# Optimization experiments

Hardware: AMD Instinct MI355X
Metric: run time of the kernel (lower is better)

## Reference

```python
import jax, jax.numpy as jnp
import numpy as np

B, N, C_IN = 8, 2048, 64
NUM_TERMS, NUM_CHANNELS = 3, 64
LN_EPS = 1e-5


def setup_inputs() -> dict:
    key = jax.random.key(0)
    k1, k2, k3 = jax.random.split(key, 3)
    A = jax.random.normal(k1, (B, N, N), dtype=jnp.float32) / jnp.sqrt(N).astype(jnp.float32)
    X = jax.random.normal(k2, (B, N, C_IN), dtype=jnp.float32)
    # xavier_uniform on h of shape [num_terms+1, num_channels, num_nodes]
    fan_in, fan_out = NUM_CHANNELS, N
    bound = float(np.sqrt(6.0 / (fan_in + fan_out)))
    h = jax.random.uniform(k3, (NUM_TERMS + 1, NUM_CHANNELS, N), dtype=jnp.float32,
                           minval=-bound, maxval=bound)
    gamma = jnp.ones((NUM_CHANNELS,), dtype=jnp.float32)
    beta = jnp.zeros((NUM_CHANNELS,), dtype=jnp.float32)
    return {"A": A, "X": X, "h": h, "gamma": gamma, "beta": beta}


def reference(A, X, h, gamma, beta):
    # Original loops compute: Y[b,n,c] = sum_i h[i,c,n] * (A^i @ sum_ch X[...,ch])[b,n]
    num_terms = h.shape[0] - 1
    Xs = X.sum(axis=-1)  # [B, N] -- inner channel loop collapses to a sum

    def step(p, _):
        p_next = jnp.einsum('bmn,bn->bm', A, p)  # A^i @ Xs
        return p_next, p_next

    _, Ps = jax.lax.scan(step, Xs, None, length=num_terms)  # [T, B, N]
    P = jnp.concatenate([Xs[None], Ps], axis=0)  # [T+1, B, N], P[0] = I @ Xs

    Y = jnp.einsum('icn,ibn->bnc', h, P)  # [B, N, C]

    mean = Y.mean(axis=-1, keepdims=True)
    var = Y.var(axis=-1, keepdims=True)
    Yn = (Y - mean) * jax.lax.rsqrt(var + LN_EPS) * gamma + beta
    return jnp.tanh(Yn)
```

## Files before the change

### kernel.cpp

```cpp
#include <hip/hip_runtime.h>
#include <hip/hip_bf16.h>
#include <hip/hip_fp16.h>
#include <math.h>

#define BB 8
#define NN 2048
#define C_IN 64
#define NCH 64
#define LN_EPS 1e-5f

__global__ void xsum_kernel(const float* __restrict__ X, float* __restrict__ Xs) {
    int row  = (blockIdx.x * blockDim.x + threadIdx.x) >> 6;
    int lane = threadIdx.x & 63;
    float v = X[(size_t)row * C_IN + lane];
    #pragma unroll
    for (int off = 32; off > 0; off >>= 1)
        v += __shfl_down(v, off, 64);
    if (lane == 0) Xs[row] = v;
}

__global__ __launch_bounds__(256, 4) void matvec_cvt_kernel(
        const float* __restrict__ A,
        const float* __restrict__ pin,
        float* __restrict__ pout,
        __half* __restrict__ A16) {
    const int b    = blockIdx.y;
    const int wave = threadIdx.x >> 6;
    const int lane = threadIdx.x & 63;
    const int m    = blockIdx.x * 4 + wave;

    const float4* pin4 = (const float4*)(pin + (size_t)b * NN);
    const float4* Ar   = (const float4*)(A + (size_t)b * NN * NN + (size_t)m * NN);

    float4 x[8], pr[8];
    #pragma unroll
    for (int j = 0; j < 8; ++j) x[j]  = Ar[j * 64 + lane];
    #pragma unroll
    for (int j = 0; j < 8; ++j) pr[j] = pin4[j * 64 + lane];

    float acc = 0.f;
    #pragma unroll
    for (int j = 0; j < 8; ++j)
        acc += x[j].x * pr[j].x + x[j].y * pr[j].y + x[j].z * pr[j].z + x[j].w * pr[j].w;

    float2* A16r = (float2*)(A16 + (size_t)b * NN * NN + (size_t)m * NN);
    #pragma unroll
    for (int j = 0; j < 8; ++j) {
        union { float2 f2; __half2 h2[2]; } u;
        u.h2[0] = __floats2half2_rn(x[j].x, x[j].y);
        u.h2[1] = __floats2half2_rn(x[j].z, x[j].w);
        A16r[j * 64 + lane] = u.f2;
    }

    #pragma unroll
    for (int off = 32; off > 0; off >>= 1)
        acc += __shfl_down(acc, off, 64);
    if (lane == 0) pout[(size_t)b * NN + m] = acc;
}

__global__ __launch_bounds__(256, 4) void matvec16_kernel(
        const __half* __restrict__ A16,
        const float* __restrict__ pin,
        float* __restrict__ pout) {
    const int b    = blockIdx.y;
    const int wave = threadIdx.x >> 6;
    const int lane = threadIdx.x & 63;
    const int m    = blockIdx.x * 4 + wave;

    const float4* pin4 = (const float4*)(pin + (size_t)b * NN);
    const float4* Ar   = (const float4*)(A16 + (size_t)b * NN * NN + (size_t)m * NN);

    float4 xr[4], pa[4], pb[4];
    #pragma unroll
    for (int j = 0; j < 4; ++j) xr[j] = Ar[j * 64 + lane];
    #pragma unroll
    for (int j = 0; j < 4; ++j) {
        pa[j] = pin4[2 * (j * 64 + lane)];
        pb[j] = pin4[2 * (j * 64 + lane) + 1];
    }

    float acc = 0.f;
    #pragma unroll
    for (int j = 0; j < 4; ++j) {
        const __half2* hx = (const __half2*)&xr[j];
        float2 f0 = __half22float2(hx[0]);
        float2 f1 = __half22float2(hx[1]);
        float2 f2 = __half22float2(hx[2]);
        float2 f3 = __half22float2(hx[3]);
        acc += f0.x * pa[j].x + f0.y * pa[j].y + f1.x * pa[j].z + f1.y * pa[j].w
             + f2.x * pb[j].x + f2.y * pb[j].y + f3.x * pb[j].z + f3.y * pb[j].w;
    }

    #pragma unroll
    for (int off = 32; off > 0; off >>= 1)
        acc += __shfl_down(acc, off, 64);
    if (lane == 0) pout[(size_t)b * NN + m] = acc;
}

__global__ __launch_bounds__(256, 4) void matvec16_ln_kernel(
        const __half* __restrict__ A16,
        const float* __restrict__ P,
        const float* __restrict__ h,
        const float* __restrict__ gamma,
        const float* __restrict__ beta,
        float* __restrict__ out) {
    const int b    = blockIdx.y;
    const int wave = threadIdx.x >> 6;
    const int lane = threadIdx.x & 63;
    const int n    = blockIdx.x * 4 + wave;

    const float4* pin4 = (const float4*)(P + (size_t)(2 * BB + b) * NN);
    const float4* Ar   = (const float4*)(A16 + (size_t)b * NN * NN + (size_t)n * NN);

    float4 xr[4], pa[4], pb[4];
    #pragma unroll
    for (int j = 0; j < 4; ++j) xr[j] = Ar[j * 64 + lane];
    #pragma unroll
    for (int j = 0; j < 4; ++j) {
        pa[j] = pin4[2 * (j * 64 + lane)];
        pb[j] = pin4[2 * (j * 64 + lane) + 1];
    }

    float acc = 0.f;
    #pragma unroll
    for (int j = 0; j < 4; ++j) {
        const __half2* hx = (const __half2*)&xr[j];
        float2 f0 = __half22float2(hx[0]);
        float2 f1 = __half22float2(hx[1]);
        float2 f2 = __half22float2(hx[2]);
        float2 f3 = __half22float2(hx[3]);
        acc += f0.x * pa[j].x + f0.y * pa[j].y + f1.x * pa[j].z + f1.y * pa[j].w
             + f2.x * pb[j].x + f2.y * pb[j].y + f3.x * pb[j].z + f3.y * pb[j].w;
    }
    #pragma unroll
    for (int off = 32; off > 0; off >>= 1)
        acc += __shfl_xor(acc, off, 64);
    const float p3 = acc;

    const int idx = b * NN + n;
    const float p0 = P[idx];
    const float p1 = P[BB * NN + idx];
    const float p2 = P[2 * BB * NN + idx];

    float y = h[(size_t)(0 * NCH + lane) * NN + n] * p0
            + h[(size_t)(1 * NCH + lane) * NN + n] * p1
            + h[(size_t)(2 * NCH + lane) * NN + n] * p2
            + h[(size_t)(3 * NCH + lane) * NN + n] * p3;

    float s = y;
    #pragma unroll
    for (int off = 32; off > 0; off >>= 1)
        s += __shfl_xor(s, off, 64);
    const float mean = s * (1.f / NCH);

    float d = y - mean;
    float vs = d * d;
    #pragma unroll
    for (int off = 32; off > 0; off >>= 1)
        vs += __shfl_xor(vs, off, 64);
    const float rstd = rsqrtf(vs * (1.f / NCH) + LN_EPS);

    out[(size_t)idx * NCH + lane] = tanhf(d * rstd * gamma[lane] + beta[lane]);
}

extern "C" void kernel_launch(void* const* d_in, const int* in_sizes, int n_in,
                              void* d_out, int out_size, void* d_ws, size_t ws_size,
                              hipStream_t stream) {
    const float* A     = (const float*)d_in[0];
    const float* X     = (const float*)d_in[1];
    const float* h     = (const float*)d_in[2];
    const float* gamma = (const float*)d_in[3];
    const float* beta  = (const float*)d_in[4];
    float* out = (float*)d_out;

    float*  P   = (float*)d_ws;
    __half* A16 = (__half*)((char*)d_ws + (1u << 20));

    dim3 mv_grid(NN / 4, BB);

    xsum_kernel<<<(BB * NN) / 4, 256, 0, stream>>>(X, P);

    matvec_cvt_kernel<<<mv_grid, 256, 0, stream>>>(A, P, P + BB * NN, A16);

    matvec16_kernel<<<mv_grid, 256, 0, stream>>>(
        A16, P + BB * NN, P + 2 * BB * NN);

    matvec16_ln_kernel<<<mv_grid, 256, 0, stream>>>(
        A16, P, h, gamma, beta, out);
}
```

Baseline: 247.0 us.

## Stage input vector in LDS and process four rows per wave with prefetch

Each block now loads the per-batch input vector once into shared memory and each wave handles four matrix rows instead of one, double-buffering the next row's loads in registers while computing the current one. The goal is to cut redundant global reads of the vector, which every wave previously fetched for itself, and to keep more memory requests in flight per wave. The cost is a quarter as many blocks in the grid, more registers per thread, and one block-wide sync.

```diff
diff --git a/kernel.cpp b/kernel.cpp
--- a/kernel.cpp
+++ b/kernel.cpp
@@ -24,77 +24,111 @@
         const float* __restrict__ pin,
         float* __restrict__ pout,
         __half* __restrict__ A16) {
-    const int b    = blockIdx.y;
+    __shared__ float4 p4[NN / 4];
+    const int b = blockIdx.y;
+
+    const float4* src = (const float4*)(pin + (size_t)b * NN);
+    p4[threadIdx.x]       = src[threadIdx.x];
+    p4[threadIdx.x + 256] = src[threadIdx.x + 256];
+    __syncthreads();
+
     const int wave = threadIdx.x >> 6;
     const int lane = threadIdx.x & 63;
-    const int m    = blockIdx.x * 4 + wave;
-
-    const float4* pin4 = (const float4*)(pin + (size_t)b * NN);
-    const float4* Ar   = (const float4*)(A + (size_t)b * NN * NN + (size_t)m * NN);
-
-    float4 x[8], pr[8];
-    #pragma unroll
-    for (int j = 0; j < 8; ++j) x[j]  = Ar[j * 64 + lane];
-    #pragma unroll
-    for (int j = 0; j < 8; ++j) pr[j] = pin4[j * 64 + lane];
-
-    float acc = 0.f;
-    #pragma unroll
-    for (int j = 0; j < 8; ++j)
-        acc += x[j].x * pr[j].x + x[j].y * pr[j].y + x[j].z * pr[j].z + x[j].w * pr[j].w;
-
-    float2* A16r = (float2*)(A16 + (size_t)b * NN * NN + (size_t)m * NN);
-    #pragma unroll
-    for (int j = 0; j < 8; ++j) {
-        union { float2 f2; __half2 h2[2]; } u;
-        u.h2[0] = __floats2half2_rn(x[j].x, x[j].y);
-        u.h2[1] = __floats2half2_rn(x[j].z, x[j].w);
-        A16r[j * 64 + lane] = u.f2;
-    }
-
-    #pragma unroll
-    for (int off = 32; off > 0; off >>= 1)
-        acc += __shfl_down(acc, off, 64);
-    if (lane == 0) pout[(size_t)b * NN + m] = acc;
+    const int m0   = blockIdx.x * 16 + wave * 4;
+    const float* Ab = A + (size_t)b * NN * NN;
+
+    float4 buf[2][8];
+    {
+        const float4* r = (const float4*)(Ab + (size_t)m0 * NN);
+        #pragma unroll
+        for (int j = 0; j < 8; ++j) buf[0][j] = r[j * 64 + lane];
+    }
+
+    #pragma unroll
+    for (int i = 0; i < 4; ++i) {
+        const int m = m0 + i;
+        if (i < 3) {
+            const float4* rn = (const float4*)(Ab + (size_t)(m + 1) * NN);
+            #pragma unroll
+            for (int j = 0; j < 8; ++j) buf[(i + 1) & 1][j] = rn[j * 64 + lane];
+        }
+
+        float acc = 0.f;
+        #pragma unroll
+        for (int j = 0; j < 8; ++j) {
+            float4 x  = buf[i & 1][j];
+            float4 pv = p4[j * 64 + lane];
+            acc += x.x * pv.x + x.y * pv.y + x.z * pv.z + x.w * pv.w;
+        }
+
+        float2* A16r = (float2*)(A16 + (size_t)b * NN * NN + (size_t)m * NN);
+        #pragma unroll
+        for (int j = 0; j < 8; ++j) {
+            union { float2 f2; __half2 h2[2]; } u;
+            u.h2[0] = __floats2half2_rn(buf[i & 1][j].x, buf[i & 1][j].y);
+            u.h2[1] = __floats2half2_rn(buf[i & 1][j].z, buf[i & 1][j].w);
+            A16r[j * 64 + lane] = u.f2;
+        }
+
+        #pragma unroll
+        for (int off = 32; off > 0; off >>= 1)
+            acc += __shfl_down(acc, off, 64);
+        if (lane == 0) pout[(size_t)b * NN + m] = acc;
+    }
 }
 
 __global__ __launch_bounds__(256, 4) void matvec16_kernel(
         const __half* __restrict__ A16,
         const float* __restrict__ pin,
         float* __restrict__ pout) {
-    const int b    = blockIdx.y;
+    __shared__ float4 p4[NN / 4];
+    const int b = blockIdx.y;
+
+    const float4* src = (const float4*)(pin + (size_t)b * NN);
+    p4[threadIdx.x]       = src[threadIdx.x];
+    p4[threadIdx.x + 256] = src[threadIdx.x + 256];
+    __syncthreads();
+
     const int wave = threadIdx.x >> 6;
     const int lane = threadIdx.x & 63;
-    const int m    = blockIdx.x * 4 + wave;
-
-    const float4* pin4 = (const float4*)(pin + (size_t)b * NN);
-    const float4* Ar   = (const float4*)(A16 + (size_t)b * NN * NN + (size_t)m * NN);
-
-    float4 xr[4], pa[4], pb[4];
-    #pragma unroll
-    for (int j = 0; j < 4; ++j) xr[j] = Ar[j * 64 + lane];
-    #pragma unroll
-    for (int j = 0; j < 4; ++j) {
-        pa[j] = pin4[2 * (j * 64 + lane)];
-        pb[j] = pin4[2 * (j * 64 + lane) + 1];
-    }
-
-    float acc = 0.f;
-    #pragma unroll
-    for (int j = 0; j < 4; ++j) {
-        const __half2* hx = (const __half2*)&xr[j];
-        float2 f0 = __half22float2(hx[0]);
-        float2 f1 = __half22float2(hx[1]);
-        float2 f2 = __half22float2(hx[2]);
-        float2 f3 = __half22float2(hx[3]);
-        acc += f0.x * pa[j].x + f0.y * pa[j].y + f1.x * pa[j].z + f1.y * pa[j].w
-             + f2.x * pb[j].x + f2.y * pb[j].y + f3.x * pb[j].z + f3.y * pb[j].w;
-    }
-
-    #pragma unroll
-    for (int off = 32; off > 0; off >>= 1)
-        acc += __shfl_down(acc, off, 64);
-    if (lane == 0) pout[(size_t)b * NN + m] = acc;
+    const int m0   = blockIdx.x * 16 + wave * 4;
+    const __half* Ab = A16 + (size_t)b * NN * NN;
+
+    float4 buf[2][4];
+    {
+        const float4* r = (const float4*)(Ab + (size_t)m0 * NN);
+        #pragma unroll
+        for (int j = 0; j < 4; ++j) buf[0][j] = r[j * 64 + lane];
+    }
+
+    #pragma unroll
+    for (int i = 0; i < 4; ++i) {
+        const int m = m0 + i;
+        if (i < 3) {
+            const float4* rn = (const float4*)(Ab + (size_t)(m + 1) * NN);
+            #pragma unroll
+            for (int j = 0; j < 4; ++j) buf[(i + 1) & 1][j] = rn[j * 64 + lane];
+        }
+
+        float acc = 0.f;
+        #pragma unroll
+        for (int j = 0; j < 4; ++j) {
+            float4 pa = p4[2 * (j * 64 + lane)];
+            float4 pb = p4[2 * (j * 64 + lane) + 1];
+            const __half2* hx = (const __half2*)&buf[i & 1][j];
+            float2 f0 = __half22float2(hx[0]);
+            float2 f1 = __half22float2(hx[1]);
+            float2 f2 = __half22float2(hx[2]);
+            float2 f3 = __half22float2(hx[3]);
+            acc += f0.x * pa.x + f0.y * pa.y + f1.x * pa.z + f1.y * pa.w
+                 + f2.x * pb.x + f2.y * pb.y + f3.x * pb.z + f3.y * pb.w;
+        }
+
+        #pragma unroll
+        for (int off = 32; off > 0; off >>= 1)
+            acc += __shfl_down(acc, off, 64);
+        if (lane == 0) pout[(size_t)b * NN + m] = acc;
+    }
 }
 
 __global__ __launch_bounds__(256, 4) void matvec16_ln_kernel(
@@ -104,63 +138,78 @@
         const float* __restrict__ gamma,
         const float* __restrict__ beta,
         float* __restrict__ out) {
-    const int b    = blockIdx.y;
+    __shared__ float4 p4[NN / 4];
+    const int b = blockIdx.y;
+
+    const float4* src = (const float4*)(P + (size_t)(2 * BB + b) * NN);
+    p4[threadIdx.x]       = src[threadIdx.x];
+    p4[threadIdx.x + 256] = src[threadIdx.x + 256];
+    __syncthreads();
+
     const int wave = threadIdx.x >> 6;
     const int lane = threadIdx.x & 63;
-    const int n    = blockIdx.x * 4 + wave;
-
-    const float4* pin4 = (const float4*)(P + (size_t)(2 * BB + b) * NN);
-    const float4* Ar   = (const float4*)(A16 + (size_t)b * NN * NN + (size_t)n * NN);
-
-    float4 xr[4], pa[4], pb[4];
-    #pragma unroll
-    for (int j = 0; j < 4; ++j) xr[j] = Ar[j * 64 + lane];
-    #pragma unroll
-    for (int j = 0; j < 4; ++j) {
-        pa[j] = pin4[2 * (j * 64 + lane)];
-        pb[j] = pin4[2 * (j * 64 + lane) + 1];
-    }
-
-    float acc = 0.f;
-    #pragma unroll
-    for (int j = 0; j < 4; ++j) {
-        const __half2* hx = (const __half2*)&xr[j];
-        float2 f0 = __half22float2(hx[0]);
-        float2 f1 = __half22float2(hx[1]);
-        float2 f2 = __half22float2(hx[2]);
-        float2 f3 = __half22float2(hx[3]);
-        acc += f0.x * pa[j].x + f0.y * pa[j].y + f1.x * pa[j].z + f1.y * pa[j].w
-             + f2.x * pb[j].x + f2.y * pb[j].y + f3.x * pb[j].z + f3.y * pb[j].w;
-    }
-    #pragma unroll
-    for (int off = 32; off > 0; off >>= 1)
-        acc += __shfl_xor(acc, off, 64);
-    const float p3 = acc;
-
-    const int idx = b * NN + n;
-    const float p0 = P[idx];
-    const float p1 = P[BB * NN + idx];
-    const float p2 = P[2 * BB * NN + idx];
-
-    float y = h[(size_t)(0 * NCH + lane) * NN + n] * p0
-            + h[(size_t)(1 * NCH + lane) * NN + n] * p1
-            + h[(size_t)(2 * NCH + lane) * NN + n] * p2
-            + h[(size_t)(3 * NCH + lane) * NN + n] * p3;
-
-    float s = y;
-    #pragma unroll
-    for (int off = 32; off > 0; off >>= 1)
-        s += __shfl_xor(s, off, 64);
-    const float mean = s * (1.f / NCH);
-
-    float d = y - mean;
-    float vs = d * d;
-    #pragma unroll
-    for (int off = 32; off > 0; off >>= 1)
-        vs += __shfl_xor(vs, off, 64);
-    const float rstd = rsqrtf(vs * (1.f / NCH) + LN_EPS);
-
-    out[(size_t)idx * NCH + lane] = tanhf(d * rstd * gamma[lane] + beta[lane]);
+    const int m0   = blockIdx.x * 16 + wave * 4;
+    const __half* Ab = A16 + (size_t)b * NN * NN;
+
+    float4 buf[2][4];
+    {
+        const float4* r = (const float4*)(Ab + (size_t)m0 * NN);
+        #pragma unroll
+        for (int j = 0; j < 4; ++j) buf[0][j] = r[j * 64 + lane];
+    }
+
+    #pragma unroll
+    for (int i = 0; i < 4; ++i) {
+        const int m = m0 + i;
+        if (i < 3) {
+            const float4* rn = (const float4*)(Ab + (size_t)(m + 1) * NN);
+            #pragma unroll
+            for (int j = 0; j < 4; ++j) buf[(i + 1) & 1][j] = rn[j * 64 + lane];
+        }
+
+        float acc = 0.f;
+        #pragma unroll
+        for (int j = 0; j < 4; ++j) {
+            float4 pa = p4[2 * (j * 64 + lane)];
+            float4 pb = p4[2 * (j * 64 + lane) + 1];
+            const __half2* hx = (const __half2*)&buf[i & 1][j];
+            float2 f0 = __half22float2(hx[0]);
+            float2 f1 = __half22float2(hx[1]);
+            float2 f2 = __half22float2(hx[2]);
+            float2 f3 = __half22float2(hx[3]);
+            acc += f0.x * pa.x + f0.y * pa.y + f1.x * pa.z + f1.y * pa.w
+                 + f2.x * pb.x + f2.y * pb.y + f3.x * pb.z + f3.y * pb.w;
+        }
+        #pragma unroll
+        for (int off = 32; off > 0; off >>= 1)
+            acc += __shfl_xor(acc, off, 64);
+        const float p3 = acc;
+
+        const int idx = b * NN + m;
+        const float p0 = P[idx];
+        const float p1 = P[BB * NN + idx];
+        const float p2 = ((const float*)p4)[m & (NN - 1)];
+
+        float y = h[(size_t)(0 * NCH + lane) * NN + m] * p0
+                + h[(size_t)(1 * NCH + lane) * NN + m] * p1
+                + h[(size_t)(2 * NCH + lane) * NN + m] * p2
+                + h[(size_t)(3 * NCH + lane) * NN + m] * p3;
+
+        float s = y;
+        #pragma unroll
+        for (int off = 32; off > 0; off >>= 1)
+            s += __shfl_xor(s, off, 64);
+        const float mean = s * (1.f / NCH);
+
+        float d = y - mean;
+        float vs = d * d;
+        #pragma unroll
+        for (int off = 32; off > 0; off >>= 1)
+            vs += __shfl_xor(vs, off, 64);
+        const float rstd = rsqrtf(vs * (1.f / NCH) + LN_EPS);
+
+        out[(size_t)idx * NCH + lane] = tanhf(d * rstd * gamma[lane] + beta[lane]);
+    }
 }
 
 extern "C" void kernel_launch(void* const* d_in, const int* in_sizes, int n_in,
@@ -176,7 +225,7 @@
     float*  P   = (float*)d_ws;
     __half* A16 = (__half*)((char*)d_ws + (1u << 20));
 
-    dim3 mv_grid(NN / 4, BB);
+    dim3 mv_grid(NN / 16, BB);
 
     xsum_kernel<<<(BB * NN) / 4, 256, 0, stream>>>(X, P);
 
```

After: 246.2 us. No clear change (-0.3%).
